# Optimization experiments

Hardware: AMD Instinct MI355X
Metric: run time of the kernel (lower is better)

## Reference

```python
import jax, jax.numpy as jnp
import numpy as np

B, T, D, F, H = 512, 48, 128, 16, 512


def setup_inputs() -> dict:
    key = jax.random.key(0)
    ks = jax.random.split(key, 7)
    return {
        "input": jax.random.normal(ks[0], (B, T, D, F), dtype=jnp.float32),
        "attn_w": jax.random.normal(ks[1], (2 * H + F * T,), dtype=jnp.float32) * 0.02,
        "attn_b": jax.random.normal(ks[2], (1,), dtype=jnp.float32) * 0.02,
        "w_ih": jax.random.normal(ks[3], (4 * H, D * F), dtype=jnp.float32) * 0.02,
        "w_hh": jax.random.normal(ks[4], (4 * H, H), dtype=jnp.float32) * 0.02,
        "b_ih": jax.random.normal(ks[5], (4 * H,), dtype=jnp.float32) * 0.02,
        "b_hh": jax.random.normal(ks[6], (4 * H,), dtype=jnp.float32) * 0.02,
    }


def reference(input, attn_w, attn_b, w_ih, w_hh, b_ih, b_hh):
    Bsz, Ts, Dn, Fn = input.shape
    Hs = w_hh.shape[1]
    # permute(0,2,3,1): [B, T, D, F] -> [B, D, F, T]
    x_perm = jnp.transpose(input, (0, 2, 3, 1))
    x_flat = x_perm.reshape(Bsz, Dn, Fn * Ts)  # [B, D, F*T]
    # encode_attn input is concat(hidden, cell, x); split the weight accordingly
    w_h, w_c, w_x = attn_w[:Hs], attn_w[Hs:2 * Hs], attn_w[2 * Hs:]
    # x contribution to attention logits is constant across steps
    e_x = x_flat @ w_x + attn_b[0]             # [B, D]
    xs = jnp.moveaxis(x_perm, 3, 0)            # [T, B, D, F] (time-major for scan)
    bias = b_ih + b_hh                         # fuse the two LSTM biases

    def step(carry, x_t):
        h, c = carry                           # [B, H] each
        e = e_x + (h @ w_h)[:, None] + (c @ w_c)[:, None]  # [B, D]
        a = jax.nn.softmax(e, axis=-1)
        x_hat = (a[:, :, None] * x_t).reshape(Bsz, Dn * Fn)  # [B, D*F]
        gates = x_hat @ w_ih.T + h @ w_hh.T + bias            # [B, 4H]
        i, f, g, o = jnp.split(gates, 4, axis=-1)  # torch LSTM gate order
        c_new = jax.nn.sigmoid(f) * c + jax.nn.sigmoid(i) * jnp.tanh(g)
        h_new = jax.nn.sigmoid(o) * jnp.tanh(c_new)
        return (h_new, c_new), h_new

    h0 = jnp.zeros((Bsz, Hs), dtype=input.dtype)
    _, hs = jax.lax.scan(step, (h0, h0), xs)   # hs: [T, B, H]
    return jnp.transpose(hs, (1, 0, 2))        # [B, T, H] == hidden_states[:, 1:]
```

## Files before the change

### kernel.cpp

```cpp
#include <hip/hip_runtime.h>

#define B_ 512
#define T_ 48
#define D_ 128
#define F_ 16
#define H_ 512

typedef float f32x4 __attribute__((ext_vector_type(4)));
typedef short s16x8 __attribute__((ext_vector_type(8)));
typedef unsigned short u16x8 __attribute__((ext_vector_type(8)));
typedef unsigned short u16x4 __attribute__((ext_vector_type(4)));
typedef unsigned long long u64;

__device__ __forceinline__ unsigned short f2bf(float x) {
  unsigned u = __float_as_uint(x);
  u += 0x7fffu + ((u >> 16) & 1u);
  return (unsigned short)(u >> 16);
}
__device__ __forceinline__ float bf2f(unsigned short h) {
  return __uint_as_float(((unsigned)h) << 16);
}
__device__ __forceinline__ float fsig(float x) {
  float e = __builtin_amdgcn_exp2f(-1.442695041f * x);
  return __builtin_amdgcn_rcpf(1.f + e);
}
__device__ __forceinline__ float ftanh(float x) {
  float e = __builtin_amdgcn_exp2f(2.885390082f * x);
  return 1.f - 2.f * __builtin_amdgcn_rcpf(1.f + e);
}

__device__ __forceinline__ void st_sys_u64(u64* p, u64 v) {
  __hip_atomic_store(p, v, __ATOMIC_RELAXED, __HIP_MEMORY_SCOPE_SYSTEM);
}
__device__ __forceinline__ u64 ld_sys_u64(const u64* p) {
  return __hip_atomic_load((u64*)p, __ATOMIC_RELAXED, __HIP_MEMORY_SCOPE_SYSTEM);
}
__device__ __forceinline__ void st_sys_u16(unsigned short* p, unsigned short v) {
  __hip_atomic_store(p, v, __ATOMIC_RELAXED, __HIP_MEMORY_SCOPE_SYSTEM);
}
__device__ __forceinline__ void st_sys_u32(unsigned* p, unsigned v) {
  __hip_atomic_store(p, v, __ATOMIC_RELAXED, __HIP_MEMORY_SCOPE_SYSTEM);
}
__device__ __forceinline__ unsigned ld_sys_u32(const unsigned* p) {
  return __hip_atomic_load((unsigned*)p, __ATOMIC_RELAXED, __HIP_MEMORY_SCOPE_SYSTEM);
}

#define AS1 __attribute__((address_space(1)))
#define AS3 __attribute__((address_space(3)))
__device__ __forceinline__ void g2lds16(const void* g, void* l) {
  __builtin_amdgcn_global_load_lds((const AS1 void*)g, (AS3 void*)l, 16, 0, 0);
}

__global__ __launch_bounds__(256) void k_prep(const float* __restrict__ wih,
                                              const float* __restrict__ whh,
                                              unsigned short* __restrict__ wih_b,
                                              unsigned short* __restrict__ whh_b) {
  long i4 = ((long)blockIdx.x * 256 + threadIdx.x) * 4;
  if (i4 < 4194304) {
    float4 v = *(const float4*)(wih + i4);
    u16x4 o = {f2bf(v.x), f2bf(v.y), f2bf(v.z), f2bf(v.w)};
    *(u16x4*)(wih_b + i4) = o;
  } else {
    long j = i4 - 4194304;
    if (j < 1048576) {
      float4 v = *(const float4*)(whh + j);
      u16x4 o = {f2bf(v.x), f2bf(v.y), f2bf(v.z), f2bf(v.w)};
      *(u16x4*)(whh_b + j) = o;
    }
  }
}

__global__ __launch_bounds__(256) void k_ex(const float* __restrict__ in,
                                            const float* __restrict__ attn_w,
                                            const float* __restrict__ attn_b,
                                            float* __restrict__ a_out) {
  __shared__ float wx[768];
  __shared__ float red2[256];
  __shared__ float red[128];
  const int b = blockIdx.x, tid = threadIdx.x;
  const int d = tid & 127, half = tid >> 7;
  for (int i = tid; i < 768; i += 256) wx[i] = attn_w[1024 + i];
  __syncthreads();
  const float* base = in + (long)b * 98304 + (long)d * 16;
  float acc = 0.f;
  for (int t = half * 24; t < half * 24 + 24; ++t) {
    const float4* p = (const float4*)(base + (long)t * 2048);
    float4 v0 = p[0], v1 = p[1], v2 = p[2], v3 = p[3];
    acc += v0.x * wx[t]       + v0.y * wx[48 + t]  + v0.z * wx[96 + t]  + v0.w * wx[144 + t];
    acc += v1.x * wx[192 + t] + v1.y * wx[240 + t] + v1.z * wx[288 + t] + v1.w * wx[336 + t];
    acc += v2.x * wx[384 + t] + v2.y * wx[432 + t] + v2.z * wx[480 + t] + v2.w * wx[528 + t];
    acc += v3.x * wx[576 + t] + v3.y * wx[624 + t] + v3.z * wx[672 + t] + v3.w * wx[720 + t];
  }
  red2[tid] = acc;
  __syncthreads();
  float a2 = 0.f;
  if (tid < 128) {
    a2 = red2[tid] + red2[tid + 128] + attn_b[0];
    red[tid] = a2;
  }
  __syncthreads();
  for (int s = 64; s > 0; s >>= 1) {
    if (tid < s) red[tid] = fmaxf(red[tid], red[tid + s]);
    __syncthreads();
  }
  float mx = red[0];
  __syncthreads();
  float ex = 0.f;
  if (tid < 128) {
    ex = expf(a2 - mx);
    red[tid] = ex;
  }
  __syncthreads();
  for (int s = 64; s > 0; s >>= 1) {
    if (tid < s) red[tid] += red[tid + s];
    __syncthreads();
  }
  if (tid < 128) a_out[b * 128 + d] = ex / red[0];
}

__global__ __launch_bounds__(256) void k_xhat(const float* __restrict__ in,
                                              const float* __restrict__ a,
                                              unsigned short* __restrict__ xh) {
  const int mrow = blockIdx.x;
  const int t = mrow >> 9, b = mrow & 511;
  const int tid = threadIdx.x;
  const int k = tid * 8;
  const int d = k >> 4;
  const int f0 = k & 15;
  const float* src = in + (((long)(b * 48 + t) * 128 + d) * 16 + f0);
  float4 v0 = *(const float4*)src;
  float4 v1 = *(const float4*)(src + 4);
  float s = a[b * 128 + d];
  u16x8 o;
  o[0] = f2bf(v0.x * s); o[1] = f2bf(v0.y * s); o[2] = f2bf(v0.z * s); o[3] = f2bf(v0.w * s);
  o[4] = f2bf(v1.x * s); o[5] = f2bf(v1.y * s); o[6] = f2bf(v1.z * s); o[7] = f2bf(v1.w * s);
  *(u16x8*)(xh + (long)mrow * 2048 + k) = o;
}


#define G_STAGE(ktv, s)                                                         \
  do {                                                                          \
    const long ko_ = (long)(ktv) * 64 + (long)(s) * 262144;                     \
    char* la_ = (char*)SM + ((ktv) & 1) * 32768 + (s) * 16384 + ldsw;           \
    g2lds16(Ag + ko_, la_);                                                     \
    g2lds16(Ag + ko_ + 131072, la_ + 8192);                                     \
    g2lds16(Bg + ko_, la_ + 65536);                                             \
    g2lds16(Bg + ko_ + 131072, la_ + 73728);                                    \
  } while (0)

#define G_LDA4(dst, bufel, ksv, mh)                                             \
  do {                                                                          \
    const unsigned short* ab_ =                                                 \
        SM + (bufel) + aBase + (mh) * 4096 + (psw ^ ((ksv) * 32));              \
    dst[0] = *(const s16x8*)(ab_);                                              \
    dst[1] = *(const s16x8*)(ab_ + 1024);                                       \
    dst[2] = *(const s16x8*)(ab_ + 2048);                                       \
    dst[3] = *(const s16x8*)(ab_ + 3072);                                       \
  } while (0)

#define G_LDB4(dst, bufel, ksv)                                                 \
  do {                                                                          \
    const unsigned short* bb_ = SM + (bufel) + bBase + (psw ^ ((ksv) * 32));    \
    dst[0] = *(const s16x8*)(bb_);                                              \
    dst[1] = *(const s16x8*)(bb_ + 1024);                                       \
    dst[2] = *(const s16x8*)(bb_ + 2048);                                       \
    dst[3] = *(const s16x8*)(bb_ + 3072);                                       \
  } while (0)

#define G_MMA2(mh, Af, Bf)                                                      \
  do {                                                                          \
    __builtin_amdgcn_s_setprio(1);                                              \
    _Pragma("unroll") for (int mt_ = 0; mt_ < 4; ++mt_)                         \
        _Pragma("unroll") for (int nt_ = 0; nt_ < 4; ++nt_)                     \
            acc[(mh) * 4 + mt_][nt_] = __builtin_amdgcn_mfma_f32_16x16x32_bf16( \
                Af[mt_], Bf[nt_], acc[(mh) * 4 + mt_][nt_], 0, 0, 0);           \
    __builtin_amdgcn_s_setprio(0);                                              \
  } while (0)

#define G_GATE(n) asm volatile("s_waitcnt vmcnt(" #n ")" ::: "memory")

__global__ __launch_bounds__(512, 2) void k_gemm(const unsigned short* __restrict__ A,
                                                 const unsigned short* __restrict__ Bw,
                                                 unsigned short* __restrict__ C) {
  __shared__ __align__(16) unsigned short SM[65536];
  const int tid = threadIdx.x;
  const int w = tid >> 6, lane = tid & 63;
  const int q = lane >> 4, l16 = lane & 15;
  const int wm = w >> 2, wn = w & 3;
  const int id = blockIdx.x;
  const int xcd = id & 7, j = id >> 3;
  const long m0 = ((long)xcd * 12 + (j >> 3)) * 256;
  const long n0 = (long)(j & 7) * 256;

  const int srow = w * 8 + (lane >> 3);
  const int csrc = (lane & 7) ^ (lane >> 3);
  const unsigned short* Ag = A + (m0 + srow) * 2048 + csrc * 8;
  const unsigned short* Bg = Bw + (n0 + srow) * 2048 + csrc * 8;
  const int ldsw = w * 1024;

  const int psw = (q ^ (l16 & 7)) * 8;
  const int aBase = (wm * 128 + l16) * 64;
  const int bBase = 32768 + (wn * 64 + l16) * 64;

  f32x4 acc[8][4];
  const f32x4 zz = {0.f, 0.f, 0.f, 0.f};
#pragma unroll
  for (int i = 0; i < 8; ++i)
#pragma unroll
    for (int j2 = 0; j2 < 4; ++j2) acc[i][j2] = zz;

  G_STAGE(0, 0);
  G_STAGE(0, 1);
  G_GATE(0);
  __builtin_amdgcn_s_barrier();

#pragma unroll 1
  for (int kt = 0; kt < 31; ++kt) {
    const int bufel = (kt & 1) * 16384;
    s16x8 b0[4], b1[4], a00[4], a01[4], a10[4], a11[4];
    G_LDB4(b0, bufel, 0);
    G_LDA4(a00, bufel, 0, 0);
    G_STAGE(kt + 1, 0);
    G_LDA4(a01, bufel, 0, 1);
    G_STAGE(kt + 1, 1);
    G_MMA2(0, a00, b0);
    G_LDB4(b1, bufel, 1);
    G_LDA4(a10, bufel, 1, 0);
    G_MMA2(1, a01, b0);
    G_LDA4(a11, bufel, 1, 1);
    G_MMA2(0, a10, b1);
    G_MMA2(1, a11, b1);
    G_GATE(0);
    __builtin_amdgcn_s_barrier();
  }
  {
    s16x8 b0[4], b1[4], a00[4], a01[4], a10[4], a11[4];
    G_LDB4(b0, 16384, 0);
    G_LDA4(a00, 16384, 0, 0);
    G_LDA4(a01, 16384, 0, 1);
    G_MMA2(0, a00, b0);
    G_LDB4(b1, 16384, 1);
    G_LDA4(a10, 16384, 1, 0);
    G_MMA2(1, a01, b0);
    G_LDA4(a11, 16384, 1, 1);
    G_MMA2(0, a10, b1);
    G_MMA2(1, a11, b1);
  }

#pragma unroll
  for (int mh = 0; mh < 2; ++mh)
#pragma unroll
    for (int mt = 0; mt < 4; ++mt)
#pragma unroll
      for (int nt = 0; nt < 4; ++nt)
#pragma unroll
        for (int r = 0; r < 4; ++r) {
          long m = m0 + wm * 128 + mh * 64 + mt * 16 + q * 4 + r;
          long n = n0 + wn * 64 + nt * 16 + l16;
          C[m * 2048 + n] = f2bf(acc[mh * 4 + mt][nt][r]);
        }
}

__global__ __launch_bounds__(256, 1) void k_rec(const unsigned short* __restrict__ gx,
                                                const unsigned short* __restrict__ whh_b,
                                                const float* __restrict__ b_ih,
                                                const float* __restrict__ b_hh,
                                                unsigned short* __restrict__ h_buf,
                                                float* __restrict__ out,
                                                unsigned int* __restrict__ bar) {
  __shared__ __align__(16) float slab[16 * 32 * 36];
  __shared__ __align__(16) unsigned short hs_own[32 * 40];
  const int tid = threadIdx.x;
  const int w = tid >> 6, lane = tid & 63;
  const int q = lane >> 4, l16 = lane & 15;
  const int bt = blockIdx.x & 15, g = blockIdx.x >> 4;
  const int b0 = bt * 32;
  const int pj = tid & 31;
  const int pr0 = (tid >> 5) * 4;
  unsigned int* slots = &bar[bt * 16];
  const int ownw = ((g >> 2) == w);
  const int ownc = g & 3;

  s16x8 wreg[32];
#pragma unroll
  for (int quad = 0; quad < 4; ++quad)
#pragma unroll
    for (int nt = 0; nt < 2; ++nt)
#pragma unroll
      for (int ci = 0; ci < 4; ++ci) {
        const unsigned short* wp =
            whh_b + (long)(quad * 512 + g * 32 + nt * 16 + l16) * 512 + (w * 4 + ci) * 32 + q * 8;
        asm volatile("global_load_dwordx4 %0, %1, off"
                     : "=v"(wreg[(quad * 2 + nt) * 4 + ci]) : "v"(wp) : "memory");
      }
  asm volatile("s_waitcnt vmcnt(0)" ::: "memory");
  __builtin_amdgcn_sched_barrier(0);

  float bias_[4];
#pragma unroll
  for (int qq = 0; qq < 4; ++qq) {
    int jj = qq * 512 + g * 32 + pj;
    bias_[qq] = b_ih[jj] + b_hh[jj];
  }
  float creg[4] = {0.f, 0.f, 0.f, 0.f};
  const f32x4 zz = {0.f, 0.f, 0.f, 0.f};

#define LD_CHUNK(slot, ci)                                                      \
  do {                                                                          \
    long o_ = hbase + (w * 4 + (ci)) * 8;                                       \
    L[slot][0] = ld_sys_u64(hb + o_);                                           \
    L[slot][1] = ld_sys_u64(hb + o_ + 1);                                       \
    L[slot][2] = ld_sys_u64(hb + o_ + 2048);                                    \
    L[slot][3] = ld_sys_u64(hb + o_ + 2049);                                    \
  } while (0)

  for (int t = 0; t < 48; ++t) {
    unsigned short gxr[4][4];
    const unsigned short* gp = gx + ((long)t * 512 + b0 + pr0) * 2048 + g * 32 + pj;
#pragma unroll
    for (int rr = 0; rr < 4; ++rr)
#pragma unroll
      for (int qq = 0; qq < 4; ++qq)
        gxr[qq][rr] = gp[rr * 2048 + qq * 512];

    if (t > 0) {
      const int need = (lane < 4) && !(ownw && lane == ownc);
      const unsigned* fp = &slots[w * 4 + (lane & 3)];
      while (1) {
        unsigned v = need ? ld_sys_u32(fp) : 0xffffffffu;
        if (__all((int)(v >= (unsigned)t))) break;
      }
      u64 L[2][4];
      const u64* hb = (const u64*)(h_buf + ((t - 1) & 1) * (512 * 512));
      const long hbase = (long)(b0 + l16) * 128 + q * 2;
      f32x4 acc[4][2][2];
#pragma unroll
      for (int a = 0; a < 4; ++a)
#pragma unroll
        for (int b = 0; b < 2; ++b)
#pragma unroll
          for (int c = 0; c < 2; ++c) acc[a][b][c] = zz;
      if (!(ownw && 0 == ownc)) LD_CHUNK(0, 0);
#pragma unroll
      for (int ci = 0; ci < 4; ++ci) {
        if (ci < 3 && !(ownw && (ci + 1) == ownc)) LD_CHUNK((ci + 1) & 1, ci + 1);
        s16x8 af0, af1;
        if (ownw && ci == ownc) {
          af0 = *(const s16x8*)&hs_own[l16 * 40 + q * 8];
          af1 = *(const s16x8*)&hs_own[(16 + l16) * 40 + q * 8];
        } else {
          union { u64 u[2]; s16x8 v; } c0, c1;
          c0.u[0] = L[ci & 1][0]; c0.u[1] = L[ci & 1][1];
          c1.u[0] = L[ci & 1][2]; c1.u[1] = L[ci & 1][3];
          af0 = c0.v; af1 = c1.v;
        }
#pragma unroll
        for (int quad = 0; quad < 4; ++quad)
#pragma unroll
          for (int nt = 0; nt < 2; ++nt) {
            acc[quad][nt][0] = __builtin_amdgcn_mfma_f32_16x16x32_bf16(
                af0, wreg[(quad * 2 + nt) * 4 + ci], acc[quad][nt][0], 0, 0, 0);
            acc[quad][nt][1] = __builtin_amdgcn_mfma_f32_16x16x32_bf16(
                af1, wreg[(quad * 2 + nt) * 4 + ci], acc[quad][nt][1], 0, 0, 0);
          }
      }
#pragma unroll
      for (int quad = 0; quad < 4; ++quad)
#pragma unroll
        for (int nt = 0; nt < 2; ++nt)
#pragma unroll
          for (int mh = 0; mh < 2; ++mh)
            *(f32x4*)&slab[((w * 4 + quad) * 32 + nt * 16 + l16) * 36 + mh * 16 + q * 4] =
                acc[quad][nt][mh];
    }
    __syncthreads();

    float hval[4];
    {
      f32x4 gs[4];
      if (t > 0) {
#pragma unroll
        for (int qq = 0; qq < 4; ++qq) {
          f32x4 s0 = *(const f32x4*)&slab[((0 * 4 + qq) * 32 + pj) * 36 + pr0];
          f32x4 s1 = *(const f32x4*)&slab[((1 * 4 + qq) * 32 + pj) * 36 + pr0];
          f32x4 s2 = *(const f32x4*)&slab[((2 * 4 + qq) * 32 + pj) * 36 + pr0];
          f32x4 s3 = *(const f32x4*)&slab[((3 * 4 + qq) * 32 + pj) * 36 + pr0];
          gs[qq] = (s0 + s1) + (s2 + s3);
        }
      } else {
#pragma unroll
        for (int qq = 0; qq < 4; ++qq) gs[qq] = zz;
      }
#pragma unroll
      for (int rr = 0; rr < 4; ++rr) {
        float g0 = gs[0][rr] + bias_[0] + bf2f(gxr[0][rr]);
        float g1 = gs[1][rr] + bias_[1] + bf2f(gxr[1][rr]);
        float g2 = gs[2][rr] + bias_[2] + bf2f(gxr[2][rr]);
        float g3 = gs[3][rr] + bias_[3] + bf2f(gxr[3][rr]);
        float is = fsig(g0);
        float fs = fsig(g1);
        float gt = ftanh(g2);
        float os = fsig(g3);
        creg[rr] = fs * creg[rr] + is * gt;
        hval[rr] = os * ftanh(creg[rr]);
      }
    }
#pragma unroll
    for (int rr = 0; rr < 4; ++rr) {
      unsigned short hb16 = f2bf(hval[rr]);
      hs_own[(pr0 + rr) * 40 + pj] = hb16;
      st_sys_u16(&h_buf[(t & 1) * (512 * 512) + (b0 + pr0 + rr) * 512 + g * 32 + pj], hb16);
    }
    __syncthreads();
    if (t < 47 && tid == 0)
      st_sys_u32(&slots[g], (unsigned)(t + 1));
#pragma unroll
    for (int rr = 0; rr < 4; ++rr)
      __builtin_nontemporal_store(
          hval[rr], &out[(long)(b0 + pr0 + rr) * (T_ * H_) + (long)t * H_ + g * 32 + pj]);
  }
#undef LD_CHUNK
}

extern "C" void kernel_launch(void* const* d_in, const int* in_sizes, int n_in,
                              void* d_out, int out_size, void* d_ws, size_t ws_size,
                              hipStream_t stream) {
  const float* input  = (const float*)d_in[0];
  const float* attn_w = (const float*)d_in[1];
  const float* attn_b = (const float*)d_in[2];
  const float* w_ih   = (const float*)d_in[3];
  const float* w_hh   = (const float*)d_in[4];
  const float* b_ih   = (const float*)d_in[5];
  const float* b_hh   = (const float*)d_in[6];
  float* out = (float*)d_out;

  char* ws = (char*)d_ws;
  unsigned int* bar     = (unsigned int*)ws;
  float* a_ws           = (float*)(ws + 1024);
  unsigned short* h_buf = (unsigned short*)(ws + 263168);
  unsigned short* whh_b = (unsigned short*)(ws + 1311744);
  unsigned short* wih_b = (unsigned short*)(ws + 3408896);
  unsigned short* x_hat = (unsigned short*)(ws + 11797504);
  unsigned short* gxws  = (unsigned short*)(ws + 112460800);

  (void)hipMemsetAsync(d_ws, 0, 1024, stream);
  hipLaunchKernelGGL(k_prep, dim3(5120), dim3(256), 0, stream, w_ih, w_hh, wih_b, whh_b);
  hipLaunchKernelGGL(k_ex, dim3(512), dim3(256), 0, stream, input, attn_w, attn_b, a_ws);
  hipLaunchKernelGGL(k_xhat, dim3(24576), dim3(256), 0, stream, input, a_ws, x_hat);
  hipLaunchKernelGGL(k_gemm, dim3(768), dim3(512), 0, stream, x_hat, wih_b, gxws);
  hipLaunchKernelGGL(k_rec, dim3(256), dim3(256), 0, stream, gxws, whh_b, b_ih, b_hh, h_buf, out, bar);
}
```

Before: 741.0 us.

## Split attention-logit kernel and vectorize recurrent kernel h/gate/output accesses

The attention logit computation is split into a 2048-block partial-sum kernel plus a small softmax kernel, giving more parallelism for streaming the input. In the recurrent kernel, the epilogue thread mapping is transposed so each thread owns four consecutive hidden units. Gate-input loads, h_buf stores (one 64-bit atomic store instead of four 16-bit ones) and output stores become vector accesses, with the LDS slab padded to 37 to avoid bank conflicts. All four h chunks are now loaded up front instead of double-buffered, which raises register pressure and adds an extra kernel launch.

```diff
diff --git a/kernel.cpp b/kernel.cpp
--- a/kernel.cpp
+++ b/kernel.cpp
@@ -34,9 +34,6 @@
 }
 __device__ __forceinline__ u64 ld_sys_u64(const u64* p) {
   return __hip_atomic_load((u64*)p, __ATOMIC_RELAXED, __HIP_MEMORY_SCOPE_SYSTEM);
-}
-__device__ __forceinline__ void st_sys_u16(unsigned short* p, unsigned short v) {
-  __hip_atomic_store(p, v, __ATOMIC_RELAXED, __HIP_MEMORY_SCOPE_SYSTEM);
 }
 __device__ __forceinline__ void st_sys_u32(unsigned* p, unsigned v) {
   __hip_atomic_store(p, v, __ATOMIC_RELAXED, __HIP_MEMORY_SCOPE_SYSTEM);
@@ -70,52 +67,52 @@
   }
 }
 
-__global__ __launch_bounds__(256) void k_ex(const float* __restrict__ in,
-                                            const float* __restrict__ attn_w,
-                                            const float* __restrict__ attn_b,
-                                            float* __restrict__ a_out) {
+__global__ __launch_bounds__(256) void k_ex1(const float* __restrict__ in,
+                                             const float* __restrict__ attn_w,
+                                             float* __restrict__ e_part) {
   __shared__ float wx[768];
-  __shared__ float red2[256];
-  __shared__ float red[128];
-  const int b = blockIdx.x, tid = threadIdx.x;
-  const int d = tid & 127, half = tid >> 7;
+  const int bc = blockIdx.x;
+  const int b = bc >> 2, c = bc & 3;
+  const int tid = threadIdx.x;
+  const int d = tid >> 1, fh = tid & 1;
   for (int i = tid; i < 768; i += 256) wx[i] = attn_w[1024 + i];
   __syncthreads();
-  const float* base = in + (long)b * 98304 + (long)d * 16;
+  const float* base = in + (long)b * 98304 + (long)d * 16 + fh * 8;
   float acc = 0.f;
-  for (int t = half * 24; t < half * 24 + 24; ++t) {
+  for (int t = c * 12; t < c * 12 + 12; ++t) {
     const float4* p = (const float4*)(base + (long)t * 2048);
-    float4 v0 = p[0], v1 = p[1], v2 = p[2], v3 = p[3];
-    acc += v0.x * wx[t]       + v0.y * wx[48 + t]  + v0.z * wx[96 + t]  + v0.w * wx[144 + t];
-    acc += v1.x * wx[192 + t] + v1.y * wx[240 + t] + v1.z * wx[288 + t] + v1.w * wx[336 + t];
-    acc += v2.x * wx[384 + t] + v2.y * wx[432 + t] + v2.z * wx[480 + t] + v2.w * wx[528 + t];
-    acc += v3.x * wx[576 + t] + v3.y * wx[624 + t] + v3.z * wx[672 + t] + v3.w * wx[720 + t];
-  }
-  red2[tid] = acc;
-  __syncthreads();
-  float a2 = 0.f;
-  if (tid < 128) {
-    a2 = red2[tid] + red2[tid + 128] + attn_b[0];
-    red[tid] = a2;
-  }
+    float4 v0 = p[0], v1 = p[1];
+    const float* wt = wx + fh * 384 + t;
+    acc += v0.x * wt[0]   + v0.y * wt[48]  + v0.z * wt[96]  + v0.w * wt[144];
+    acc += v1.x * wt[192] + v1.y * wt[240] + v1.z * wt[288] + v1.w * wt[336];
+  }
+  acc += __shfl_xor(acc, 1);
+  if (fh == 0) e_part[(long)bc * 128 + d] = acc;
+}
+
+__global__ __launch_bounds__(128) void k_ex2(const float* __restrict__ e_part,
+                                             const float* __restrict__ attn_b,
+                                             float* __restrict__ a_out) {
+  __shared__ float red[128];
+  const int b = blockIdx.x, d = threadIdx.x;
+  float acc = attn_b[0];
+  for (int c = 0; c < 4; ++c) acc += e_part[(long)(b * 4 + c) * 128 + d];
+  red[d] = acc;
   __syncthreads();
   for (int s = 64; s > 0; s >>= 1) {
-    if (tid < s) red[tid] = fmaxf(red[tid], red[tid + s]);
+    if (d < s) red[d] = fmaxf(red[d], red[d + s]);
     __syncthreads();
   }
   float mx = red[0];
   __syncthreads();
-  float ex = 0.f;
-  if (tid < 128) {
-    ex = expf(a2 - mx);
-    red[tid] = ex;
-  }
+  float ex = expf(acc - mx);
+  red[d] = ex;
   __syncthreads();
   for (int s = 64; s > 0; s >>= 1) {
-    if (tid < s) red[tid] += red[tid + s];
+    if (d < s) red[d] += red[d + s];
     __syncthreads();
   }
-  if (tid < 128) a_out[b * 128 + d] = ex / red[0];
+  a_out[b * 128 + d] = ex / red[0];
 }
 
 __global__ __launch_bounds__(256) void k_xhat(const float* __restrict__ in,
@@ -268,15 +265,15 @@
                                                 unsigned short* __restrict__ h_buf,
                                                 float* __restrict__ out,
                                                 unsigned int* __restrict__ bar) {
-  __shared__ __align__(16) float slab[16 * 32 * 36];
+  __shared__ __align__(16) float slab[16 * 32 * 37];
   __shared__ __align__(16) unsigned short hs_own[32 * 40];
   const int tid = threadIdx.x;
   const int w = tid >> 6, lane = tid & 63;
   const int q = lane >> 4, l16 = lane & 15;
   const int bt = blockIdx.x & 15, g = blockIdx.x >> 4;
   const int b0 = bt * 32;
-  const int pj = tid & 31;
-  const int pr0 = (tid >> 5) * 4;
+  const int pm = tid >> 3;
+  const int pr0 = (tid & 7) * 4;
   unsigned int* slots = &bar[bt * 16];
   const int ownw = ((g >> 2) == w);
   const int ownc = g & 3;
@@ -296,32 +293,22 @@
   asm volatile("s_waitcnt vmcnt(0)" ::: "memory");
   __builtin_amdgcn_sched_barrier(0);
 
-  float bias_[4];
-#pragma unroll
-  for (int qq = 0; qq < 4; ++qq) {
-    int jj = qq * 512 + g * 32 + pj;
-    bias_[qq] = b_ih[jj] + b_hh[jj];
-  }
+  float bias_[16];
+#pragma unroll
+  for (int qq = 0; qq < 4; ++qq)
+#pragma unroll
+    for (int rr = 0; rr < 4; ++rr) {
+      int jj = qq * 512 + g * 32 + pr0 + rr;
+      bias_[qq * 4 + rr] = b_ih[jj] + b_hh[jj];
+    }
   float creg[4] = {0.f, 0.f, 0.f, 0.f};
   const f32x4 zz = {0.f, 0.f, 0.f, 0.f};
 
-#define LD_CHUNK(slot, ci)                                                      \
-  do {                                                                          \
-    long o_ = hbase + (w * 4 + (ci)) * 8;                                       \
-    L[slot][0] = ld_sys_u64(hb + o_);                                           \
-    L[slot][1] = ld_sys_u64(hb + o_ + 1);                                       \
-    L[slot][2] = ld_sys_u64(hb + o_ + 2048);                                    \
-    L[slot][3] = ld_sys_u64(hb + o_ + 2049);                                    \
-  } while (0)
-
   for (int t = 0; t < 48; ++t) {
-    unsigned short gxr[4][4];
-    const unsigned short* gp = gx + ((long)t * 512 + b0 + pr0) * 2048 + g * 32 + pj;
-#pragma unroll
-    for (int rr = 0; rr < 4; ++rr)
-#pragma unroll
-      for (int qq = 0; qq < 4; ++qq)
-        gxr[qq][rr] = gp[rr * 2048 + qq * 512];
+    u16x4 gxr[4];
+    const unsigned short* gp = gx + ((long)t * 512 + b0 + pm) * 2048 + g * 32 + pr0;
+#pragma unroll
+    for (int qq = 0; qq < 4; ++qq) gxr[qq] = *(const u16x4*)(gp + qq * 512);
 
     if (t > 0) {
       const int need = (lane < 4) && !(ownw && lane == ownc);
@@ -330,9 +317,19 @@
         unsigned v = need ? ld_sys_u32(fp) : 0xffffffffu;
         if (__all((int)(v >= (unsigned)t))) break;
       }
-      u64 L[2][4];
+      u64 L[4][4];
       const u64* hb = (const u64*)(h_buf + ((t - 1) & 1) * (512 * 512));
       const long hbase = (long)(b0 + l16) * 128 + q * 2;
+#pragma unroll
+      for (int ci = 0; ci < 4; ++ci) {
+        if (!(ownw && ci == ownc)) {
+          long o_ = hbase + (w * 4 + ci) * 8;
+          L[ci][0] = ld_sys_u64(hb + o_);
+          L[ci][1] = ld_sys_u64(hb + o_ + 1);
+          L[ci][2] = ld_sys_u64(hb + o_ + 2048);
+          L[ci][3] = ld_sys_u64(hb + o_ + 2049);
+        }
+      }
       f32x4 acc[4][2][2];
 #pragma unroll
       for (int a = 0; a < 4; ++a)
@@ -340,18 +337,16 @@
         for (int b = 0; b < 2; ++b)
 #pragma unroll
           for (int c = 0; c < 2; ++c) acc[a][b][c] = zz;
-      if (!(ownw && 0 == ownc)) LD_CHUNK(0, 0);
 #pragma unroll
       for (int ci = 0; ci < 4; ++ci) {
-        if (ci < 3 && !(ownw && (ci + 1) == ownc)) LD_CHUNK((ci + 1) & 1, ci + 1);
         s16x8 af0, af1;
         if (ownw && ci == ownc) {
           af0 = *(const s16x8*)&hs_own[l16 * 40 + q * 8];
           af1 = *(const s16x8*)&hs_own[(16 + l16) * 40 + q * 8];
         } else {
           union { u64 u[2]; s16x8 v; } c0, c1;
-          c0.u[0] = L[ci & 1][0]; c0.u[1] = L[ci & 1][1];
-          c1.u[0] = L[ci & 1][2]; c1.u[1] = L[ci & 1][3];
+          c0.u[0] = L[ci][0]; c0.u[1] = L[ci][1];
+          c1.u[0] = L[ci][2]; c1.u[1] = L[ci][3];
           af0 = c0.v; af1 = c1.v;
         }
 #pragma unroll
@@ -370,56 +365,43 @@
         for (int nt = 0; nt < 2; ++nt)
 #pragma unroll
           for (int mh = 0; mh < 2; ++mh)
-            *(f32x4*)&slab[((w * 4 + quad) * 32 + nt * 16 + l16) * 36 + mh * 16 + q * 4] =
+            *(f32x4*)&slab[((w * 4 + quad) * 32 + nt * 16 + l16) * 37 + mh * 16 + q * 4] =
                 acc[quad][nt][mh];
     }
     __syncthreads();
 
     float hval[4];
-    {
-      f32x4 gs[4];
-      if (t > 0) {
-#pragma unroll
-        for (int qq = 0; qq < 4; ++qq) {
-          f32x4 s0 = *(const f32x4*)&slab[((0 * 4 + qq) * 32 + pj) * 36 + pr0];
-          f32x4 s1 = *(const f32x4*)&slab[((1 * 4 + qq) * 32 + pj) * 36 + pr0];
-          f32x4 s2 = *(const f32x4*)&slab[((2 * 4 + qq) * 32 + pj) * 36 + pr0];
-          f32x4 s3 = *(const f32x4*)&slab[((3 * 4 + qq) * 32 + pj) * 36 + pr0];
-          gs[qq] = (s0 + s1) + (s2 + s3);
+#pragma unroll
+    for (int rr = 0; rr < 4; ++rr) {
+      float gv[4];
+#pragma unroll
+      for (int qq = 0; qq < 4; ++qq) {
+        float s = 0.f;
+        if (t > 0) {
+#pragma unroll
+          for (int ws = 0; ws < 4; ++ws)
+            s += slab[((ws * 4 + qq) * 32 + pr0 + rr) * 37 + pm];
         }
-      } else {
-#pragma unroll
-        for (int qq = 0; qq < 4; ++qq) gs[qq] = zz;
+        gv[qq] = s + bias_[qq * 4 + rr] + bf2f(gxr[qq][rr]);
       }
-#pragma unroll
-      for (int rr = 0; rr < 4; ++rr) {
-        float g0 = gs[0][rr] + bias_[0] + bf2f(gxr[0][rr]);
-        float g1 = gs[1][rr] + bias_[1] + bf2f(gxr[1][rr]);
-        float g2 = gs[2][rr] + bias_[2] + bf2f(gxr[2][rr]);
-        float g3 = gs[3][rr] + bias_[3] + bf2f(gxr[3][rr]);
-        float is = fsig(g0);
-        float fs = fsig(g1);
-        float gt = ftanh(g2);
-        float os = fsig(g3);
-        creg[rr] = fs * creg[rr] + is * gt;
-        hval[rr] = os * ftanh(creg[rr]);
-      }
+      float is = fsig(gv[0]);
+      float fs = fsig(gv[1]);
+      float gt = ftanh(gv[2]);
+      float os = fsig(gv[3]);
+      creg[rr] = fs * creg[rr] + is * gt;
+      hval[rr] = os * ftanh(creg[rr]);
     }
-#pragma unroll
-    for (int rr = 0; rr < 4; ++rr) {
-      unsigned short hb16 = f2bf(hval[rr]);
-      hs_own[(pr0 + rr) * 40 + pj] = hb16;
-      st_sys_u16(&h_buf[(t & 1) * (512 * 512) + (b0 + pr0 + rr) * 512 + g * 32 + pj], hb16);
-    }
+    u16x4 hb4 = {f2bf(hval[0]), f2bf(hval[1]), f2bf(hval[2]), f2bf(hval[3])};
+    u64 h8;
+    __builtin_memcpy(&h8, &hb4, 8);
+    st_sys_u64((u64*)&h_buf[(t & 1) * (512 * 512) + (b0 + pm) * 512 + g * 32 + pr0], h8);
+    *(u16x4*)&hs_own[pm * 40 + pr0] = hb4;
     __syncthreads();
     if (t < 47 && tid == 0)
       st_sys_u32(&slots[g], (unsigned)(t + 1));
-#pragma unroll
-    for (int rr = 0; rr < 4; ++rr)
-      __builtin_nontemporal_store(
-          hval[rr], &out[(long)(b0 + pr0 + rr) * (T_ * H_) + (long)t * H_ + g * 32 + pj]);
-  }
-#undef LD_CHUNK
+    f32x4 ov = {hval[0], hval[1], hval[2], hval[3]};
+    __builtin_nontemporal_store(ov, (f32x4*)&out[(long)(b0 + pm) * (T_ * H_) + (long)t * H_ + g * 32 + pr0]);
+  }
 }
 
 extern "C" void kernel_launch(void* const* d_in, const int* in_sizes, int n_in,
@@ -442,10 +424,12 @@
   unsigned short* wih_b = (unsigned short*)(ws + 3408896);
   unsigned short* x_hat = (unsigned short*)(ws + 11797504);
   unsigned short* gxws  = (unsigned short*)(ws + 112460800);
+  float* e_part         = (float*)x_hat;
 
   (void)hipMemsetAsync(d_ws, 0, 1024, stream);
   hipLaunchKernelGGL(k_prep, dim3(5120), dim3(256), 0, stream, w_ih, w_hh, wih_b, whh_b);
-  hipLaunchKernelGGL(k_ex, dim3(512), dim3(256), 0, stream, input, attn_w, attn_b, a_ws);
+  hipLaunchKernelGGL(k_ex1, dim3(2048), dim3(256), 0, stream, input, attn_w, e_part);
+  hipLaunchKernelGGL(k_ex2, dim3(512), dim3(128), 0, stream, e_part, attn_b, a_ws);
   hipLaunchKernelGGL(k_xhat, dim3(24576), dim3(256), 0, stream, input, a_ws, x_hat);
   hipLaunchKernelGGL(k_gemm, dim3(768), dim3(512), 0, stream, x_hat, wih_b, gxws);
   hipLaunchKernelGGL(k_rec, dim3(256), dim3(256), 0, stream, gxws, whh_b, b_ih, b_hh, h_buf, out, bar);
```

Result: slower. 771.4 us (+4.1%).
